# Kernel tuning notes

Hardware: AMD Instinct MI355X
Metric: run time of the kernel (lower is better)

The kernel has to match this reference:

```python
import jax, jax.numpy as jnp
import numpy as np

N, E, H, NUM_RBF = 50000, 800000, 32, 32
D_IN = 2 * (NUM_RBF + H)  # 128: att_src(H) + att_dst(H) + rbf(2*NUM_RBF)
LN_EPS = 1e-5


def _decompose(t):
    # irreducible decomposition of [..., 3, 3] tensor
    eye = jnp.eye(3, dtype=t.dtype)
    I = jnp.mean(jnp.diagonal(t, axis1=-2, axis2=-1), axis=-1)[..., None, None] * eye
    A = 0.5 * (t - jnp.swapaxes(t, -1, -2))
    S = 0.5 * (t + jnp.swapaxes(t, -1, -2)) - I
    return I, A, S


def _tnorm(t):
    # squared Frobenius norm over last two dims -> [..., H]
    return (t ** 2).sum((-2, -1))


def _chan_lin(t, W):
    # nn.Linear over channel dim: t [N,H,3,3], W [H_out,H_in]
    return jnp.einsum('nhij,gh->ngij', t, W)


def setup_inputs() -> dict:
    key = jax.random.key(0)
    ks = jax.random.split(key, 12)

    def lin(k, o, i):
        return (jax.random.normal(k, (o, i), jnp.float32) / np.sqrt(i)).astype(jnp.float32)

    return {
        'X': jax.random.normal(ks[0], (N, H, 3, 3), jnp.float32),
        'rbf': jax.random.normal(ks[1], (E, 2 * NUM_RBF), jnp.float32),
        'dist': jax.random.uniform(ks[2], (E,), jnp.float32),
        'src': jax.random.randint(ks[3], (E,), 0, N),
        'dst': jax.random.randint(ks[4], (E,), 0, N),
        'Ws0': lin(ks[5], H, D_IN), 'b0': jnp.zeros((H,), jnp.float32),
        'Ws1': lin(ks[6], 2 * H, H), 'b1': jnp.zeros((2 * H,), jnp.float32),
        'Ws2': lin(ks[7], 3 * H, 2 * H), 'b2': jnp.zeros((3 * H,), jnp.float32),
        'Wt': (jax.random.normal(ks[8], (6, H, H), jnp.float32) / np.sqrt(H)).astype(jnp.float32),
        'ln_w': jnp.ones((3 * H,), jnp.float32), 'ln_b': jnp.zeros((3 * H,), jnp.float32),
        'lin_w': lin(ks[9], H, 3 * H), 'lin_b': jnp.zeros((H,), jnp.float32),
    }


def reference(X, rbf, dist, src, dst, Ws0, b0, Ws1, b1, Ws2, b2, Wt, ln_w, ln_b, lin_w, lin_b):
    n = X.shape[0]
    act = jax.nn.silu

    # atom_inf branch: per-node scalar attributes from tensor norms
    I, A, S = _decompose(X)
    x = jnp.concatenate([_tnorm(I), _tnorm(A), _tnorm(S)], axis=-1)  # [N, 3H]
    mu = x.mean(-1, keepdims=True)
    var = x.var(-1, keepdims=True)
    x = (x - mu) / jnp.sqrt(var + LN_EPS) * ln_w + ln_b
    att = act(x @ lin_w.T + lin_b)  # [N, H]

    # edge features: cat(att[src], att[dst], rbf) -> scalar MLP
    e = jnp.concatenate([att[src], att[dst], rbf], axis=-1)  # [E, D_IN]
    e = act(e @ Ws0.T + b0)
    e = act(e @ Ws1.T + b1)
    e = act(e @ Ws2.T + b2)  # [E, 3H]
    C = jnp.ones_like(dist)  # original code overwrites cutoff with ones
    e = (e * C[:, None]).reshape(e.shape[0], H, 3)  # [E, H, 3]

    # normalize node tensors, decompose, per-channel linear mix
    Xn = X / (_tnorm(X) + 1.0)[..., None, None]
    I, A, S = _decompose(Xn)
    I = _chan_lin(I, Wt[0])
    A = _chan_lin(A, Wt[1])
    S = _chan_lin(S, Wt[2])
    Y = I + A + S

    # tensor message passing: gather src, scale by edge factor, scatter-sum to dst
    def mp(T, f):
        return jax.ops.segment_sum(T[src] * f[:, :, None, None], dst, num_segments=n)

    msg = mp(I, e[..., 0]) + mp(A, e[..., 1]) + mp(S, e[..., 2])

    # O(3) group
    B1 = jnp.matmul(msg, Y)
    B2 = jnp.matmul(Y, msg)
    I, A, S = _decompose(B1 + B2)

    normp1 = (_tnorm(I + A + S) + 1.0)[..., None, None]
    I, A, S = I / normp1, A / normp1, S / normp1
    I = _chan_lin(I, Wt[3])
    A = _chan_lin(A, Wt[4])
    S = _chan_lin(S, Wt[5])
    dX = I + A + S
    X_out = Xn + dX + jnp.matmul(dX, dX)  # matrix_power(dX, 2)
    return X_out, e
```

## Files before the change

kernel.cpp:

```cpp
#include <hip/hip_runtime.h>
#include <math.h>

#define HC 32
#define NODE_PER_BLK 8

typedef _Float16 half8 __attribute__((ext_vector_type(8)));
typedef float float4v __attribute__((ext_vector_type(4)));

__device__ __forceinline__ float silu_f(float x) { return x / (1.0f + __expf(-x)); }

__device__ __forceinline__ unsigned int pk2(float a, float b) {
    union { _Float16 h[2]; unsigned int u; } t;
    t.h[0] = (_Float16)a; t.h[1] = (_Float16)b;
    return t.u;
}
__device__ __forceinline__ void unpk2(unsigned int u, float& a, float& b) {
    union { unsigned int u; _Float16 h[2]; } t;
    t.u = u;
    a = (float)t.h[0]; b = (float)t.h[1];
}

__device__ __forceinline__ void recon3(const float* c, float* T) {
    T[0] = c[0] + c[4];  T[1] = c[1] + c[5];  T[2] = c[2] + c[6];
    T[3] = -c[1] + c[5]; T[4] = c[0] + c[7];  T[5] = c[3] + c[8];
    T[6] = -c[2] + c[6]; T[7] = -c[3] + c[8]; T[8] = c[0] - c[4] - c[7];
}

__global__ __launch_bounds__(1024) void zero_cnt(int* __restrict__ cnt, int N) {
    int i = blockIdx.x * 1024 + threadIdx.x;
    if (i < N) cnt[i] = 0;
}

__global__ void prep_weights(const float* __restrict__ Ws0, const float* __restrict__ Ws1,
                             const float* __restrict__ Ws2,
                             _Float16* __restrict__ wf1, _Float16* __restrict__ wf2,
                             _Float16* __restrict__ wf3) {
    int t = blockIdx.x * 256 + threadIdx.x;
    int j = t & 7;
    int lane = (t >> 3) & 63;
    int q = lane >> 4, r = lane & 15;
    if (t < 4096) {
        int fi = t >> 9, kt = fi >> 1, nt = fi & 1;
        wf1[t] = (_Float16)Ws0[(16 * nt + r) * 128 + 32 * kt + 8 * q + j];
    } else if (t < 6144) {
        int t2 = t - 4096;
        int nt = t2 >> 9;
        wf2[t2] = (_Float16)Ws1[(16 * nt + r) * 32 + 8 * q + j];
    } else if (t < 12288) {
        int t3 = t - 6144;
        int fi = t3 >> 9, kt = fi / 6, nt = fi % 6;
        wf3[t3] = (_Float16)Ws2[(16 * nt + r) * 64 + 32 * kt + 8 * q + j];
    }
}

__global__ void hist_kernel(const int* __restrict__ dst, int* __restrict__ cnt, int E) {
    int e = blockIdx.x * 256 + threadIdx.x;
    if (e < E) atomicAdd(&cnt[dst[e]], 1);
}

__global__ __launch_bounds__(1024) void scan_a(const int* __restrict__ cnt,
                                               int* __restrict__ bsum, int N) {
    __shared__ int s[1024];
    int i = blockIdx.x * 1024 + threadIdx.x;
    s[threadIdx.x] = (i < N) ? cnt[i] : 0;
    __syncthreads();
    #pragma unroll
    for (int o = 512; o; o >>= 1) {
        if (threadIdx.x < o) s[threadIdx.x] += s[threadIdx.x + o];
        __syncthreads();
    }
    if (threadIdx.x == 0) bsum[blockIdx.x] = s[0];
}

__global__ __launch_bounds__(1024) void scan_b(int* __restrict__ bsum, int nb) {
    __shared__ int s[1024];
    int v = (threadIdx.x < nb) ? bsum[threadIdx.x] : 0;
    s[threadIdx.x] = v;
    __syncthreads();
    #pragma unroll
    for (int o = 1; o < 1024; o <<= 1) {
        int t = (threadIdx.x >= o) ? s[threadIdx.x - o] : 0;
        __syncthreads();
        s[threadIdx.x] += t;
        __syncthreads();
    }
    if (threadIdx.x < nb) bsum[threadIdx.x] = s[threadIdx.x] - v;
}

__global__ __launch_bounds__(1024) void scan_c(const int* __restrict__ cnt,
                                               const int* __restrict__ bsum,
                                               int* __restrict__ off,
                                               int* __restrict__ cursor, int N) {
    __shared__ int s[1024];
    int i = blockIdx.x * 1024 + threadIdx.x;
    int v = (i < N) ? cnt[i] : 0;
    s[threadIdx.x] = v;
    __syncthreads();
    #pragma unroll
    for (int o = 1; o < 1024; o <<= 1) {
        int t = (threadIdx.x >= o) ? s[threadIdx.x - o] : 0;
        __syncthreads();
        s[threadIdx.x] += t;
        __syncthreads();
    }
    int ex = bsum[blockIdx.x] + s[threadIdx.x] - v;
    if (i < N) {
        off[i] = ex;
        cursor[i] = ex;
        if (i == N - 1) off[N] = ex + v;
    }
}

__global__ void scatter_kernel(const int* __restrict__ src, const int* __restrict__ dst,
                               int* __restrict__ cursor, int2* __restrict__ elist, int E) {
    int e = blockIdx.x * 256 + threadIdx.x;
    if (e >= E) return;
    int d = dst[e];
    int pos = atomicAdd(&cursor[d], 1);
    elist[pos] = make_int2(e, src[e]);
}

__global__ void node_prep(const float* __restrict__ X,
                          const float* __restrict__ lin_w, const float* __restrict__ lin_b,
                          const float* __restrict__ ln_w, const float* __restrict__ ln_b,
                          const float* __restrict__ Wt,
                          _Float16* __restrict__ att_h, unsigned int* __restrict__ comp_g, int N) {
    __shared__ float sX[NODE_PER_BLK][96];
    __shared__ float sC[NODE_PER_BLK][HC * 9];
    int grp = threadIdx.x >> 5;
    int lane = threadIdx.x & 31;
    int n = blockIdx.x * NODE_PER_BLK + grp;
    bool valid = (n < N);

    float m = 0, a01 = 0, a02 = 0, a12 = 0, s00 = 0, s01 = 0, s02 = 0, s11 = 0, s12 = 0;
    float tI = 0, tA = 0, tS = 0, tX = 0;
    if (valid) {
        const float* xp = X + (size_t)n * 288 + lane * 9;
        float t00 = xp[0], t01 = xp[1], t02 = xp[2];
        float t10 = xp[3], t11 = xp[4], t12 = xp[5];
        float t20 = xp[6], t21 = xp[7], t22 = xp[8];
        m = (t00 + t11 + t22) * (1.0f / 3.0f);
        a01 = 0.5f * (t01 - t10); a02 = 0.5f * (t02 - t20); a12 = 0.5f * (t12 - t21);
        s00 = t00 - m; s11 = t11 - m; float s22 = t22 - m;
        s01 = 0.5f * (t01 + t10); s02 = 0.5f * (t02 + t20); s12 = 0.5f * (t12 + t21);
        tI = 3.0f * m * m;
        tA = 2.0f * (a01 * a01 + a02 * a02 + a12 * a12);
        tS = s00 * s00 + s11 * s11 + s22 * s22 + 2.0f * (s01 * s01 + s02 * s02 + s12 * s12);
        tX = tI + tA + tS;
    }
    float lsum = tI + tA + tS;
    #pragma unroll
    for (int o = 16; o; o >>= 1) lsum += __shfl_xor(lsum, o, 32);
    float mu = lsum * (1.0f / 96.0f);
    float d0 = tI - mu, d1 = tA - mu, d2 = tS - mu;
    float lsq = d0 * d0 + d1 * d1 + d2 * d2;
    #pragma unroll
    for (int o = 16; o; o >>= 1) lsq += __shfl_xor(lsq, o, 32);
    float rstd = rsqrtf(lsq * (1.0f / 96.0f) + 1e-5f);
    if (valid) {
        sX[grp][lane]      = d0 * rstd * ln_w[lane]      + ln_b[lane];
        sX[grp][32 + lane] = d1 * rstd * ln_w[32 + lane] + ln_b[32 + lane];
        sX[grp][64 + lane] = d2 * rstd * ln_w[64 + lane] + ln_b[64 + lane];
    }
    __syncthreads();
    if (valid) {
        float acc = lin_b[lane];
        const float* wr = lin_w + lane * 96;
        #pragma unroll
        for (int k = 0; k < 96; k++) acc += wr[k] * sX[grp][k];
        att_h[(size_t)n * 32 + lane] = (_Float16)silu_f(acc);
        float inv = 1.0f / (tX + 1.0f);
        float* cc = &sC[grp][lane * 9];
        cc[0] = m * inv;
        cc[1] = a01 * inv; cc[2] = a02 * inv; cc[3] = a12 * inv;
        cc[4] = s00 * inv; cc[5] = s01 * inv; cc[6] = s02 * inv;
        cc[7] = s11 * inv; cc[8] = s12 * inv;
    }
    __syncthreads();
    if (valid) {
        float o[9];
        #pragma unroll
        for (int c = 0; c < 9; c++) o[c] = 0.0f;
        const float* w0 = Wt + lane * 32;
        const float* w1 = Wt + 1024 + lane * 32;
        const float* w2 = Wt + 2048 + lane * 32;
        #pragma unroll
        for (int h = 0; h < 32; h++) {
            float wi = w0[h], wa = w1[h], ws = w2[h];
            const float* ch = &sC[grp][h * 9];
            o[0] += wi * ch[0];
            o[1] += wa * ch[1]; o[2] += wa * ch[2]; o[3] += wa * ch[3];
            o[4] += ws * ch[4]; o[5] += ws * ch[5]; o[6] += ws * ch[6];
            o[7] += ws * ch[7]; o[8] += ws * ch[8];
        }
        unsigned int* cgp = comp_g + (size_t)n * 160 + lane;
        cgp[0]   = pk2(o[0], o[1]);
        cgp[32]  = pk2(o[2], o[3]);
        cgp[64]  = pk2(o[4], o[5]);
        cgp[96]  = pk2(o[6], o[7]);
        cgp[128] = pk2(o[8], 0.0f);
    }
}

__device__ __forceinline__ half8 cvt8v(const float* p) {
    float4 v0 = ((const float4*)p)[0];
    float4 v1 = ((const float4*)p)[1];
    half8 h;
    h[0] = (_Float16)v0.x; h[1] = (_Float16)v0.y; h[2] = (_Float16)v0.z; h[3] = (_Float16)v0.w;
    h[4] = (_Float16)v1.x; h[5] = (_Float16)v1.y; h[6] = (_Float16)v1.z; h[7] = (_Float16)v1.w;
    return h;
}

__global__ __launch_bounds__(256) void edge_mfma(
    const _Float16* __restrict__ att_h, const float* __restrict__ rbf,
    const int* __restrict__ src, const int* __restrict__ dst,
    const _Float16* __restrict__ wf1, const _Float16* __restrict__ wf2,
    const _Float16* __restrict__ wf3,
    const float* __restrict__ b0, const float* __restrict__ b1, const float* __restrict__ b2,
    float* __restrict__ e_out, int E) {
    __shared__ _Float16 hbuf[4][16][72];
    int w = threadIdx.x >> 6;
    int lane = threadIdx.x & 63;
    int q = lane >> 4, r = lane & 15;
    int ebase = blockIdx.x * 64 + w * 16;
    int er = min(ebase + r, E - 1);
    int s = src[er], d = dst[er];

    half8 a0 = ((const half8*)(att_h + (size_t)s * 32))[q];
    half8 a1 = ((const half8*)(att_h + (size_t)d * 32))[q];
    half8 a2 = cvt8v(rbf + (size_t)er * 64 + 8 * q);
    half8 a3 = cvt8v(rbf + (size_t)er * 64 + 32 + 8 * q);

    const half8* W1 = (const half8*)wf1;
    float bn0 = b0[r], bn1 = b0[16 + r];
    float4v acc10 = {bn0, bn0, bn0, bn0};
    float4v acc11 = {bn1, bn1, bn1, bn1};
    acc10 = __builtin_amdgcn_mfma_f32_16x16x32_f16(a0, W1[0 * 64 + lane], acc10, 0, 0, 0);
    acc11 = __builtin_amdgcn_mfma_f32_16x16x32_f16(a0, W1[1 * 64 + lane], acc11, 0, 0, 0);
    acc10 = __builtin_amdgcn_mfma_f32_16x16x32_f16(a1, W1[2 * 64 + lane], acc10, 0, 0, 0);
    acc11 = __builtin_amdgcn_mfma_f32_16x16x32_f16(a1, W1[3 * 64 + lane], acc11, 0, 0, 0);
    acc10 = __builtin_amdgcn_mfma_f32_16x16x32_f16(a2, W1[4 * 64 + lane], acc10, 0, 0, 0);
    acc11 = __builtin_amdgcn_mfma_f32_16x16x32_f16(a2, W1[5 * 64 + lane], acc11, 0, 0, 0);
    acc10 = __builtin_amdgcn_mfma_f32_16x16x32_f16(a3, W1[6 * 64 + lane], acc10, 0, 0, 0);
    acc11 = __builtin_amdgcn_mfma_f32_16x16x32_f16(a3, W1[7 * 64 + lane], acc11, 0, 0, 0);
    #pragma unroll
    for (int reg = 0; reg < 4; reg++) {
        hbuf[w][4 * q + reg][r]      = (_Float16)silu_f(acc10[reg]);
        hbuf[w][4 * q + reg][16 + r] = (_Float16)silu_f(acc11[reg]);
    }

    half8 ah1 = *(const half8*)&hbuf[w][r][8 * q];
    const half8* W2 = (const half8*)wf2;
    float4v acc2[4];
    #pragma unroll
    for (int nt = 0; nt < 4; nt++) {
        float bb = b1[16 * nt + r];
        acc2[nt] = (float4v){bb, bb, bb, bb};
        acc2[nt] = __builtin_amdgcn_mfma_f32_16x16x32_f16(ah1, W2[nt * 64 + lane], acc2[nt], 0, 0, 0);
    }
    #pragma unroll
    for (int nt = 0; nt < 4; nt++) {
        #pragma unroll
        for (int reg = 0; reg < 4; reg++) {
            hbuf[w][4 * q + reg][16 * nt + r] = (_Float16)silu_f(acc2[nt][reg]);
        }
    }

    half8 ah20 = *(const half8*)&hbuf[w][r][8 * q];
    half8 ah21 = *(const half8*)&hbuf[w][r][32 + 8 * q];
    const half8* W3 = (const half8*)wf3;
    float4v acc3[6];
    #pragma unroll
    for (int nt = 0; nt < 6; nt++) {
        float bb = b2[16 * nt + r];
        acc3[nt] = (float4v){bb, bb, bb, bb};
        acc3[nt] = __builtin_amdgcn_mfma_f32_16x16x32_f16(ah20, W3[nt * 64 + lane], acc3[nt], 0, 0, 0);
        acc3[nt] = __builtin_amdgcn_mfma_f32_16x16x32_f16(ah21, W3[(6 + nt) * 64 + lane], acc3[nt], 0, 0, 0);
    }
    #pragma unroll
    for (int nt = 0; nt < 6; nt++) {
        #pragma unroll
        for (int reg = 0; reg < 4; reg++) {
            int ee = ebase + 4 * q + reg;
            if (ee < E) e_out[(size_t)ee * 96 + 16 * nt + r] = silu_f(acc3[nt][reg]);
        }
    }
}

__global__ __launch_bounds__(256) void gather_final(
    const float* __restrict__ X, const unsigned int* __restrict__ comp_g,
    const float* __restrict__ e_out,
    const int* __restrict__ off, const int2* __restrict__ elist,
    const float* __restrict__ Wt, float* __restrict__ Xout, int N) {
    __shared__ float sB[NODE_PER_BLK][HC * 9];
    int grp = threadIdx.x >> 5;
    int lane = threadIdx.x & 31;
    int n = blockIdx.x * NODE_PER_BLK + grp;
    bool valid = (n < N);

    float cm[9];
    #pragma unroll
    for (int c = 0; c < 9; c++) cm[c] = 0.0f;

    if (valid) {
        int start = off[n], end = off[n + 1];
        int idx = start;
        for (; idx + 4 <= end; idx += 4) {
            int ex[4], sx[4];
            #pragma unroll
            for (int u = 0; u < 4; u++) {
                int2 es = elist[idx + u];
                ex[u] = es.x; sx[u] = es.y;
            }
            float ev[4][3];
            unsigned int cg[4][5];
            #pragma unroll
            for (int u = 0; u < 4; u++) {
                const float* ep = e_out + (size_t)ex[u] * 96 + lane * 3;
                ev[u][0] = ep[0]; ev[u][1] = ep[1]; ev[u][2] = ep[2];
                const unsigned int* cp = comp_g + (size_t)sx[u] * 160 + lane;
                cg[u][0] = cp[0]; cg[u][1] = cp[32]; cg[u][2] = cp[64];
                cg[u][3] = cp[96]; cg[u][4] = cp[128];
            }
            #pragma unroll
            for (int u = 0; u < 4; u++) {
                float c0, c1, c2, c3, c4, c5, c6, c7, c8, cz;
                unpk2(cg[u][0], c0, c1);
                unpk2(cg[u][1], c2, c3);
                unpk2(cg[u][2], c4, c5);
                unpk2(cg[u][3], c6, c7);
                unpk2(cg[u][4], c8, cz);
                float e0 = ev[u][0], e1 = ev[u][1], e2 = ev[u][2];
                cm[0] += e0 * c0;
                cm[1] += e1 * c1; cm[2] += e1 * c2; cm[3] += e1 * c3;
                cm[4] += e2 * c4; cm[5] += e2 * c5; cm[6] += e2 * c6;
                cm[7] += e2 * c7; cm[8] += e2 * c8;
            }
        }
        for (; idx < end; idx++) {
            int2 es = elist[idx];
            const float* ep = e_out + (size_t)es.x * 96 + lane * 3;
            float e0 = ep[0], e1 = ep[1], e2 = ep[2];
            const unsigned int* cp = comp_g + (size_t)es.y * 160 + lane;
            float c0, c1, c2, c3, c4, c5, c6, c7, c8, cz;
            unpk2(cp[0], c0, c1);
            unpk2(cp[32], c2, c3);
            unpk2(cp[64], c4, c5);
            unpk2(cp[96], c6, c7);
            unpk2(cp[128], c8, cz);
            cm[0] += e0 * c0;
            cm[1] += e1 * c1; cm[2] += e1 * c2; cm[3] += e1 * c3;
            cm[4] += e2 * c4; cm[5] += e2 * c5; cm[6] += e2 * c6;
            cm[7] += e2 * c7; cm[8] += e2 * c8;
        }
    }

    if (valid) {
        float cy[9], cz;
        const unsigned int* cgn = comp_g + (size_t)n * 160 + lane;
        unpk2(cgn[0], cy[0], cy[1]);
        unpk2(cgn[32], cy[2], cy[3]);
        unpk2(cgn[64], cy[4], cy[5]);
        unpk2(cgn[96], cy[6], cy[7]);
        unpk2(cgn[128], cy[8], cz);
        float M[9], Y[9];
        recon3(cm, M);
        recon3(cy, Y);
        float B[9];
        #pragma unroll
        for (int i = 0; i < 3; i++) {
            #pragma unroll
            for (int j = 0; j < 3; j++) {
                float acc = 0.0f;
                #pragma unroll
                for (int k = 0; k < 3; k++)
                    acc += M[i * 3 + k] * Y[k * 3 + j] + Y[i * 3 + k] * M[k * 3 + j];
                B[i * 3 + j] = acc;
            }
        }
        float mB = (B[0] + B[4] + B[8]) * (1.0f / 3.0f);
        float tn = 1.0f;
        #pragma unroll
        for (int i = 0; i < 9; i++) tn += B[i] * B[i];
        float itn = 1.0f / tn;
        float* bb = &sB[grp][lane * 9];
        bb[0] = mB * itn;
        bb[1] = 0.5f * (B[1] - B[3]) * itn;
        bb[2] = 0.5f * (B[2] - B[6]) * itn;
        bb[3] = 0.5f * (B[5] - B[7]) * itn;
        bb[4] = (B[0] - mB) * itn;
        bb[5] = 0.5f * (B[1] + B[3]) * itn;
        bb[6] = 0.5f * (B[2] + B[6]) * itn;
        bb[7] = (B[4] - mB) * itn;
        bb[8] = 0.5f * (B[5] + B[7]) * itn;
    }
    __syncthreads();
    if (valid) {
        float o[9];
        #pragma unroll
        for (int c = 0; c < 9; c++) o[c] = 0.0f;
        const float* w3 = Wt + 3 * 1024 + lane * 32;
        const float* w4 = Wt + 4 * 1024 + lane * 32;
        const float* w5 = Wt + 5 * 1024 + lane * 32;
        #pragma unroll
        for (int h = 0; h < 32; h++) {
            float wi = w3[h], wa = w4[h], ws = w5[h];
            const float* ch = &sB[grp][h * 9];
            o[0] += wi * ch[0];
            o[1] += wa * ch[1]; o[2] += wa * ch[2]; o[3] += wa * ch[3];
            o[4] += ws * ch[4]; o[5] += ws * ch[5]; o[6] += ws * ch[6];
            o[7] += ws * ch[7]; o[8] += ws * ch[8];
        }
        float D[9];
        recon3(o, D);
        const float* xp = X + (size_t)n * 288 + lane * 9;
        float xv[9];
        float tt = 0.0f;
        #pragma unroll
        for (int i = 0; i < 9; i++) { xv[i] = xp[i]; tt += xv[i] * xv[i]; }
        float inv = 1.0f / (tt + 1.0f);
        float P[9];
        #pragma unroll
        for (int i = 0; i < 3; i++) {
            #pragma unroll
            for (int j = 0; j < 3; j++) {
                float acc = 0.0f;
                #pragma unroll
                for (int k = 0; k < 3; k++) acc += D[i * 3 + k] * D[k * 3 + j];
                P[i * 3 + j] = acc;
            }
        }
        float* op = Xout + (size_t)n * 288 + lane * 9;
        #pragma unroll
        for (int i = 0; i < 9; i++) op[i] = xv[i] * inv + D[i] + P[i];
    }
}

extern "C" void kernel_launch(void* const* d_in, const int* in_sizes, int n_in,
                              void* d_out, int out_size, void* d_ws, size_t ws_size,
                              hipStream_t stream) {
    const float* X = (const float*)d_in[0];
    const float* rbf = (const float*)d_in[1];
    const int* src = (const int*)d_in[3];
    const int* dst = (const int*)d_in[4];
    const float* Ws0 = (const float*)d_in[5];
    const float* b0 = (const float*)d_in[6];
    const float* Ws1 = (const float*)d_in[7];
    const float* b1 = (const float*)d_in[8];
    const float* Ws2 = (const float*)d_in[9];
    const float* b2 = (const float*)d_in[10];
    const float* Wt = (const float*)d_in[11];
    const float* ln_w = (const float*)d_in[12];
    const float* ln_b = (const float*)d_in[13];
    const float* lin_w = (const float*)d_in[14];
    const float* lin_b = (const float*)d_in[15];

    int N = in_sizes[0] / 288;
    int E = in_sizes[1] / 64;

    float* Xout = (float*)d_out;
    float* e_out = (float*)d_out + (size_t)N * 288;

    _Float16* att_h = (_Float16*)d_ws;
    unsigned int* comp_g = (unsigned int*)(att_h + (size_t)N * 32);
    _Float16* wf1 = (_Float16*)(comp_g + (size_t)N * 160);
    _Float16* wf2 = wf1 + 4096;
    _Float16* wf3 = wf2 + 2048;
    int* cnt = (int*)(wf3 + 6144);
    int* off = cnt + N;
    int* cursor = off + N + 1;
    int* bsum = cursor + N + 1;
    int2* elist = (int2*)(bsum + 1026);

    int nb = (N + 1023) / 1024;

    zero_cnt<<<nb, 1024, 0, stream>>>(cnt, N);
    prep_weights<<<48, 256, 0, stream>>>(Ws0, Ws1, Ws2, wf1, wf2, wf3);
    node_prep<<<(N + NODE_PER_BLK - 1) / NODE_PER_BLK, 256, 0, stream>>>(
        X, lin_w, lin_b, ln_w, ln_b, Wt, att_h, comp_g, N);
    hist_kernel<<<(E + 255) / 256, 256, 0, stream>>>(dst, cnt, E);
    scan_a<<<nb, 1024, 0, stream>>>(cnt, bsum, N);
    scan_b<<<1, 1024, 0, stream>>>(bsum, nb);
    scan_c<<<nb, 1024, 0, stream>>>(cnt, bsum, off, cursor, N);
    scatter_kernel<<<(E + 255) / 256, 256, 0, stream>>>(src, dst, cursor, elist, E);
    edge_mfma<<<(E + 63) / 64, 256, 0, stream>>>(
        att_h, rbf, src, dst, wf1, wf2, wf3, b0, b1, b2, e_out, E);
    gather_final<<<(N + NODE_PER_BLK - 1) / NODE_PER_BLK, 256, 0, stream>>>(
        X, comp_g, e_out, off, elist, Wt, Xout, N);
}
```

Baseline: 579.8 us.

## Sort nodes by in-degree for balanced gather and deepen edge unrolling

Adds a counting sort of nodes by in-degree (histogram, scan, scatter into an order array) and makes gather_final process nodes in that order, so nodes sharing a wavefront or block have similar edge counts. The edge loop also gains an 8-wide batch before the 4-wide and scalar tails, to keep more gathers in flight. This adds three small kernels with highly contended atomics on few bins, and makes node reads and writes scattered instead of sequential.

New measurement: 862.3 us. +48.7%, slower.

```diff
diff --git a/kernel.cpp b/kernel.cpp
--- a/kernel.cpp
+++ b/kernel.cpp
@@ -26,9 +26,11 @@
     T[6] = -c[2] + c[6]; T[7] = -c[3] + c[8]; T[8] = c[0] - c[4] - c[7];
 }
 
-__global__ __launch_bounds__(1024) void zero_cnt(int* __restrict__ cnt, int N) {
+__global__ __launch_bounds__(1024) void zero_cnt(int* __restrict__ cnt, int N,
+                                                 int* __restrict__ dbin) {
     int i = blockIdx.x * 1024 + threadIdx.x;
     if (i < N) cnt[i] = 0;
+    if (blockIdx.x == 0 && threadIdx.x < 256) dbin[threadIdx.x] = 0;
 }
 
 __global__ void prep_weights(const float* __restrict__ Ws0, const float* __restrict__ Ws1,
@@ -120,6 +122,35 @@
     elist[pos] = make_int2(e, src[e]);
 }
 
+__global__ void deg_hist(const int* __restrict__ cnt, int* __restrict__ dbin, int N) {
+    int i = blockIdx.x * 256 + threadIdx.x;
+    if (i < N) atomicAdd(&dbin[min(cnt[i], 255)], 1);
+}
+
+__global__ __launch_bounds__(256) void deg_scan(const int* __restrict__ dbin,
+                                                int* __restrict__ dcur) {
+    __shared__ int s[256];
+    int v = dbin[threadIdx.x];
+    s[threadIdx.x] = v;
+    __syncthreads();
+    #pragma unroll
+    for (int o = 1; o < 256; o <<= 1) {
+        int t = (threadIdx.x >= o) ? s[threadIdx.x - o] : 0;
+        __syncthreads();
+        s[threadIdx.x] += t;
+        __syncthreads();
+    }
+    dcur[threadIdx.x] = s[threadIdx.x] - v;
+}
+
+__global__ void order_scatter(const int* __restrict__ cnt, int* __restrict__ dcur,
+                              int* __restrict__ order, int N) {
+    int i = blockIdx.x * 256 + threadIdx.x;
+    if (i >= N) return;
+    int pos = atomicAdd(&dcur[min(cnt[i], 255)], 1);
+    order[pos] = i;
+}
+
 __global__ void node_prep(const float* __restrict__ X,
                           const float* __restrict__ lin_w, const float* __restrict__ lin_b,
                           const float* __restrict__ ln_w, const float* __restrict__ ln_b,
@@ -287,16 +318,55 @@
     }
 }
 
+template<int U>
+__device__ __forceinline__ void gather_batch(
+    const int2* __restrict__ elist, int idx,
+    const float* __restrict__ e_out, const unsigned int* __restrict__ comp_g,
+    int lane, float* cm) {
+    int ex[U], sx[U];
+    #pragma unroll
+    for (int u = 0; u < U; u++) {
+        int2 es = elist[idx + u];
+        ex[u] = es.x; sx[u] = es.y;
+    }
+    float ev[U][3];
+    unsigned int cg[U][5];
+    #pragma unroll
+    for (int u = 0; u < U; u++) {
+        const float* ep = e_out + (size_t)ex[u] * 96 + lane * 3;
+        ev[u][0] = ep[0]; ev[u][1] = ep[1]; ev[u][2] = ep[2];
+        const unsigned int* cp = comp_g + (size_t)sx[u] * 160 + lane;
+        cg[u][0] = cp[0]; cg[u][1] = cp[32]; cg[u][2] = cp[64];
+        cg[u][3] = cp[96]; cg[u][4] = cp[128];
+    }
+    #pragma unroll
+    for (int u = 0; u < U; u++) {
+        float c0, c1, c2, c3, c4, c5, c6, c7, c8, cz;
+        unpk2(cg[u][0], c0, c1);
+        unpk2(cg[u][1], c2, c3);
+        unpk2(cg[u][2], c4, c5);
+        unpk2(cg[u][3], c6, c7);
+        unpk2(cg[u][4], c8, cz);
+        float e0 = ev[u][0], e1 = ev[u][1], e2 = ev[u][2];
+        cm[0] += e0 * c0;
+        cm[1] += e1 * c1; cm[2] += e1 * c2; cm[3] += e1 * c3;
+        cm[4] += e2 * c4; cm[5] += e2 * c5; cm[6] += e2 * c6;
+        cm[7] += e2 * c7; cm[8] += e2 * c8;
+    }
+}
+
 __global__ __launch_bounds__(256) void gather_final(
     const float* __restrict__ X, const unsigned int* __restrict__ comp_g,
     const float* __restrict__ e_out,
     const int* __restrict__ off, const int2* __restrict__ elist,
+    const int* __restrict__ order,
     const float* __restrict__ Wt, float* __restrict__ Xout, int N) {
     __shared__ float sB[NODE_PER_BLK][HC * 9];
     int grp = threadIdx.x >> 5;
     int lane = threadIdx.x & 31;
-    int n = blockIdx.x * NODE_PER_BLK + grp;
-    bool valid = (n < N);
+    int oi = blockIdx.x * NODE_PER_BLK + grp;
+    bool valid = (oi < N);
+    int n = valid ? order[oi] : 0;
 
     float cm[9];
     #pragma unroll
@@ -305,54 +375,9 @@
     if (valid) {
         int start = off[n], end = off[n + 1];
         int idx = start;
-        for (; idx + 4 <= end; idx += 4) {
-            int ex[4], sx[4];
-            #pragma unroll
-            for (int u = 0; u < 4; u++) {
-                int2 es = elist[idx + u];
-                ex[u] = es.x; sx[u] = es.y;
-            }
-            float ev[4][3];
-            unsigned int cg[4][5];
-            #pragma unroll
-            for (int u = 0; u < 4; u++) {
-                const float* ep = e_out + (size_t)ex[u] * 96 + lane * 3;
-                ev[u][0] = ep[0]; ev[u][1] = ep[1]; ev[u][2] = ep[2];
-                const unsigned int* cp = comp_g + (size_t)sx[u] * 160 + lane;
-                cg[u][0] = cp[0]; cg[u][1] = cp[32]; cg[u][2] = cp[64];
-                cg[u][3] = cp[96]; cg[u][4] = cp[128];
-            }
-            #pragma unroll
-            for (int u = 0; u < 4; u++) {
-                float c0, c1, c2, c3, c4, c5, c6, c7, c8, cz;
-                unpk2(cg[u][0], c0, c1);
-                unpk2(cg[u][1], c2, c3);
-                unpk2(cg[u][2], c4, c5);
-                unpk2(cg[u][3], c6, c7);
-                unpk2(cg[u][4], c8, cz);
-                float e0 = ev[u][0], e1 = ev[u][1], e2 = ev[u][2];
-                cm[0] += e0 * c0;
-                cm[1] += e1 * c1; cm[2] += e1 * c2; cm[3] += e1 * c3;
-                cm[4] += e2 * c4; cm[5] += e2 * c5; cm[6] += e2 * c6;
-                cm[7] += e2 * c7; cm[8] += e2 * c8;
-            }
-        }
-        for (; idx < end; idx++) {
-            int2 es = elist[idx];
-            const float* ep = e_out + (size_t)es.x * 96 + lane * 3;
-            float e0 = ep[0], e1 = ep[1], e2 = ep[2];
-            const unsigned int* cp = comp_g + (size_t)es.y * 160 + lane;
-            float c0, c1, c2, c3, c4, c5, c6, c7, c8, cz;
-            unpk2(cp[0], c0, c1);
-            unpk2(cp[32], c2, c3);
-            unpk2(cp[64], c4, c5);
-            unpk2(cp[96], c6, c7);
-            unpk2(cp[128], c8, cz);
-            cm[0] += e0 * c0;
-            cm[1] += e1 * c1; cm[2] += e1 * c2; cm[3] += e1 * c3;
-            cm[4] += e2 * c4; cm[5] += e2 * c5; cm[6] += e2 * c6;
-            cm[7] += e2 * c7; cm[8] += e2 * c8;
-        }
+        for (; idx + 8 <= end; idx += 8) gather_batch<8>(elist, idx, e_out, comp_g, lane, cm);
+        for (; idx + 4 <= end; idx += 4) gather_batch<4>(elist, idx, e_out, comp_g, lane, cm);
+        for (; idx < end; idx++)         gather_batch<1>(elist, idx, e_out, comp_g, lane, cm);
     }
 
     if (valid) {
@@ -470,11 +495,14 @@
     int* off = cnt + N;
     int* cursor = off + N + 1;
     int* bsum = cursor + N + 1;
-    int2* elist = (int2*)(bsum + 1026);
+    int* dbin = bsum + 1026;
+    int* dcur = dbin + 256;
+    int* order = dcur + 256;
+    int2* elist = (int2*)(order + N + (N & 1));
 
     int nb = (N + 1023) / 1024;
 
-    zero_cnt<<<nb, 1024, 0, stream>>>(cnt, N);
+    zero_cnt<<<nb, 1024, 0, stream>>>(cnt, N, dbin);
     prep_weights<<<48, 256, 0, stream>>>(Ws0, Ws1, Ws2, wf1, wf2, wf3);
     node_prep<<<(N + NODE_PER_BLK - 1) / NODE_PER_BLK, 256, 0, stream>>>(
         X, lin_w, lin_b, ln_w, ln_b, Wt, att_h, comp_g, N);
@@ -482,9 +510,12 @@
     scan_a<<<nb, 1024, 0, stream>>>(cnt, bsum, N);
     scan_b<<<1, 1024, 0, stream>>>(bsum, nb);
     scan_c<<<nb, 1024, 0, stream>>>(cnt, bsum, off, cursor, N);
+    deg_hist<<<(N + 255) / 256, 256, 0, stream>>>(cnt, dbin, N);
+    deg_scan<<<1, 256, 0, stream>>>(dbin, dcur);
+    order_scatter<<<(N + 255) / 256, 256, 0, stream>>>(cnt, dcur, order, N);
     scatter_kernel<<<(E + 255) / 256, 256, 0, stream>>>(src, dst, cursor, elist, E);
     edge_mfma<<<(E + 63) / 64, 256, 0, stream>>>(
         att_h, rbf, src, dst, wf1, wf2, wf3, b0, b1, b2, e_out, E);
     gather_final<<<(N + NODE_PER_BLK - 1) / NODE_PER_BLK, 256, 0, stream>>>(
-        X, comp_g, e_out, off, elist, Wt, Xout, N);
-}
+        X, comp_g, e_out, off, elist, order, Wt, Xout, N);
+}
```
